# Optimization experiments

Hardware: AMD Instinct MI355X
Metric: run time of the kernel (lower is better)

The kernel has to match this reference:

```python
import jax, jax.numpy as jnp
import numpy as np

BATCH, SEQ, IN_DIM, UNITS = 32, 512, 512, 1024


def setup_inputs() -> dict:
    key = jax.random.key(0)
    k1, k2, k3 = jax.random.split(key, 3)
    data = jax.random.normal(k1, (BATCH, SEQ, IN_DIM), dtype=jnp.float32)
    Wx = jax.random.normal(k2, (IN_DIM, 4 * UNITS), dtype=jnp.float32) * 0.02
    Wh = jax.random.normal(k3, (UNITS, 4 * UNITS), dtype=jnp.float32) * 0.02
    b = jnp.zeros((4 * UNITS,), dtype=jnp.float32)
    return {"data": data, "Wx": Wx, "Wh": Wh, "b": b}


def reference(data, Wx, Wh, b):
    # Precompute input projections for all timesteps at once: [B, T, 4U]
    x_proj = jnp.einsum("bti,iu->btu", data, Wx) + b
    units = Wh.shape[0]
    B = data.shape[0]

    def step(carry, xp_t):
        h, c = carry
        gates = xp_t + h @ Wh  # [B, 4U]
        i, f, g, o = jnp.split(gates, 4, axis=-1)
        i = jax.nn.sigmoid(i)
        f = jax.nn.sigmoid(f)
        g = jnp.tanh(g)
        o = jax.nn.sigmoid(o)
        c_new = f * c + i * g
        h_new = o * jnp.tanh(c_new)
        return (h_new, c_new), h_new

    h0 = jnp.zeros((B, units), dtype=data.dtype)
    c0 = jnp.zeros((B, units), dtype=data.dtype)
    # scan over time axis: xs is [T, B, 4U]
    (_, _), hs = jax.lax.scan(step, (h0, c0), jnp.swapaxes(x_proj, 0, 1))
    # return_sequences=True -> [B, T, U]
    return jnp.swapaxes(hs, 0, 1)
```

## Files before the change

kernel.cpp:

```cpp
#include <hip/hip_runtime.h>
#include <cstdint>
#include <cstddef>

typedef __bf16 bf16x8 __attribute__((ext_vector_type(8)));
typedef __bf16 bf16x4 __attribute__((ext_vector_type(4)));
typedef float  f32x4  __attribute__((ext_vector_type(4)));

#define WS_WFRAG   0
#define WS_XB      12582912
#define WS_XCHG    29360128
#define WS_CNT     62914560
#define WS_NEEDED  62930944

#define LDS_BYTES  163840

#define SENT 0xFFFFFFFFFFFFFFFFULL

__device__ __forceinline__ void gload16(const void* g, void* l) {
    __builtin_amdgcn_global_load_lds(
        (const __attribute__((address_space(1))) void*)(g),
        (__attribute__((address_space(3))) void*)(l),
        16, 0, 0);
}

__device__ __forceinline__ float sigmoidf_(float x) {
    return 1.f / (1.f + __expf(-x));
}
__device__ __forceinline__ float tanhf_(float x) {
    x = fminf(fmaxf(x, -15.f), 15.f);
    float e2 = __expf(2.f * x);
    return (e2 - 1.f) / (e2 + 1.f);
}

__global__ void __launch_bounds__(256) prep_w_kernel(const float* __restrict__ Wx,
                                                     const float* __restrict__ Wh,
                                                     __bf16* __restrict__ wfrag) {
    int tid = blockIdx.x * 256 + threadIdx.x;
    int l   = tid & 63;
    int m   = tid >> 6;
    int nt  = m & 1;
    int sk  = m >> 1;
    int kk  = sk % 48;
    int s   = sk / 48;
    int lc  = l & 15;
    int c   = nt * 16 + lc;
    int uu  = c >> 2;
    int gi  = c & 3;
    int n   = gi * 1024 + s * 8 + uu;
    int k0  = kk * 32 + (l >> 4) * 8;
    bf16x8 v;
#pragma unroll
    for (int j = 0; j < 8; ++j) {
        int k  = k0 + j;
        float f = (k < 512) ? Wx[k * 4096 + n] : Wh[(k - 512) * 4096 + n];
        v[j] = (__bf16)f;
    }
    ((bf16x8*)wfrag)[tid] = v;
}

__global__ void __launch_bounds__(256) prep_x_kernel(const float* __restrict__ data,
                                                     __bf16* __restrict__ xb) {
    int tid = blockIdx.x * 256 + threadIdx.x;
    float4 v = ((const float4*)data)[tid];
    bf16x4 o;
    o[0] = (__bf16)v.x; o[1] = (__bf16)v.y; o[2] = (__bf16)v.z; o[3] = (__bf16)v.w;
    ((bf16x4*)xb)[tid] = o;
}

__global__ void __launch_bounds__(128)
lstm_main(const __bf16* __restrict__ xb, const __bf16* __restrict__ wfrag,
          const float* __restrict__ bias, float* __restrict__ out,
          __bf16* __restrict__ hbuf, unsigned* __restrict__ cnt) {
    extern __shared__ char smem[];
    __bf16* X_lds = (__bf16*)smem;
    __bf16* H_lds = (__bf16*)(smem + 32768);
    __bf16* W_lds = (__bf16*)(smem + 65536);

    const int tid = threadIdx.x;
    const int l   = tid & 63;
    const int w   = tid >> 6;
    const int q   = l >> 4;
    const int r   = l & 15;
    const int bid = blockIdx.x;
    const int s   = bid & 127;
    const int g   = bid >> 7;
    const int gb0 = g * 16;

    const __bf16* wsrc = wfrag + (size_t)s * 49152;
    for (int m = w * 48; m < w * 48 + 48; ++m) {
        gload16(wsrc + m * 512 + l * 8, W_lds + m * 512);
    }

    const int uu = w * 4 + q;
    const int u  = s * 8 + uu;
    const float b_i = bias[u];
    const float b_f = bias[1024 + u];
    const float b_g = bias[2048 + u];
    const float b_o = bias[3072 + u];
    float cst = 0.f;

    unsigned* fl = cnt + g * 1024;

    {
        const __bf16* xrow = xb + (size_t)(gb0 + r) * 512 * 512;
#pragma unroll
        for (int j = 0; j < 8; ++j) {
            int m = w * 8 + j;
            gload16(xrow + m * 32 + q * 8, X_lds + m * 512);
        }
    }

    __syncthreads();

    for (int t = 0; t < 512; ++t) {
        if (t > 0) {
            const unsigned tgt = (unsigned)t;
            while (__hip_atomic_load(fl + w * 64 + l, __ATOMIC_RELAXED,
                                     __HIP_MEMORY_SCOPE_AGENT) < tgt) {}
        }

        unsigned long long va[16], vb[16];
        const __bf16* hsrc = hbuf + (size_t)t * 32768 + (size_t)g * 16384;
#pragma unroll
        for (int j = 0; j < 16; ++j) {
            int m = w * 16 + j;
            ulonglong2 v = *(const ulonglong2*)(hsrc + (m * 4 + q) * 128 + r * 8);
            va[j] = v.x; vb[j] = v.y;
        }

        const __bf16* Xc = X_lds + (t & 1) * 8192;
        f32x4 acc0 = {0.f, 0.f, 0.f, 0.f};
        f32x4 acc1 = {0.f, 0.f, 0.f, 0.f};
#pragma unroll
        for (int kk = 0; kk < 16; kk += 2) {
            bf16x8 a0 = *(const bf16x8*)(Xc + kk * 512 + l * 8);
            bf16x8 b0 = *(const bf16x8*)(W_lds + (kk * 2 + w) * 512 + l * 8);
            acc0 = __builtin_amdgcn_mfma_f32_16x16x32_bf16(a0, b0, acc0, 0, 0, 0);
            bf16x8 a1 = *(const bf16x8*)(Xc + (kk + 1) * 512 + l * 8);
            bf16x8 b1 = *(const bf16x8*)(W_lds + ((kk + 1) * 2 + w) * 512 + l * 8);
            acc1 = __builtin_amdgcn_mfma_f32_16x16x32_bf16(a1, b1, acc1, 0, 0, 0);
        }

        if (t > 0) {
            for (;;) {
                int miss = 0;
#pragma unroll
                for (int j = 0; j < 16; ++j)
                    miss += (va[j] == SENT) + (vb[j] == SENT);
                if (miss == 0) break;
                __builtin_amdgcn_s_sleep(1);
#pragma unroll
                for (int j = 0; j < 16; ++j) {
                    int m = w * 16 + j;
                    const unsigned long long* p =
                        (const unsigned long long*)(hsrc + (m * 4 + q) * 128 + r * 8);
                    if (va[j] == SENT)
                        va[j] = __hip_atomic_load(p,     __ATOMIC_RELAXED, __HIP_MEMORY_SCOPE_AGENT);
                    if (vb[j] == SENT)
                        vb[j] = __hip_atomic_load(p + 1, __ATOMIC_RELAXED, __HIP_MEMORY_SCOPE_AGENT);
                }
            }
        }

#pragma unroll
        for (int j = 0; j < 16; ++j) {
            int m = w * 16 + j;
            unsigned long long tmp[2] = {va[j], vb[j]};
            *((ulonglong2*)(H_lds + m * 512 + l * 8)) = *(const ulonglong2*)tmp;
        }
        __syncthreads();

#pragma unroll 4
        for (int kk = 16; kk < 48; kk += 2) {
            bf16x8 a0 = *(const bf16x8*)(H_lds + (kk - 16) * 512 + l * 8);
            bf16x8 b0 = *(const bf16x8*)(W_lds + (kk * 2 + w) * 512 + l * 8);
            acc0 = __builtin_amdgcn_mfma_f32_16x16x32_bf16(a0, b0, acc0, 0, 0, 0);
            bf16x8 a1 = *(const bf16x8*)(H_lds + (kk - 15) * 512 + l * 8);
            bf16x8 b1 = *(const bf16x8*)(W_lds + ((kk + 1) * 2 + w) * 512 + l * 8);
            acc1 = __builtin_amdgcn_mfma_f32_16x16x32_bf16(a1, b1, acc1, 0, 0, 0);
        }

        float*  scr   = (float*)(smem + ((t + 1) & 1) * 16384);
        __bf16* hpack = (__bf16*)(smem + ((t + 1) & 1) * 16384 + 2176);
        float* sw = scr + w * 272;
#pragma unroll
        for (int rg = 0; rg < 4; ++rg) {
            sw[(l & 15) * 17 + q * 4 + rg] = acc0[rg] + acc1[rg];
        }
        float xi = sw[(q * 4 + 0) * 17 + r];
        float xf = sw[(q * 4 + 1) * 17 + r];
        float xg = sw[(q * 4 + 2) * 17 + r];
        float xo = sw[(q * 4 + 3) * 17 + r];

        float ii = sigmoidf_(xi + b_i);
        float ff = sigmoidf_(xf + b_f);
        float gg = tanhf_(xg + b_g);
        float oo = sigmoidf_(xo + b_o);
        cst = ff * cst + ii * gg;
        float h = oo * tanhf_(cst);

        const int bglob = gb0 + r;

        if (t < 511) {
            hpack[r * 8 + uu] = (__bf16)h;
            __syncthreads();
            if (w == 0) {
                if (tid < 32) {
                    unsigned long long v = ((const unsigned long long*)hpack)[tid];
                    unsigned long long* dst = (unsigned long long*)
                        (hbuf + (size_t)(t + 1) * 32768 + (size_t)g * 16384 + s * 128) + tid;
                    __hip_atomic_store(dst, v, __ATOMIC_RELAXED, __HIP_MEMORY_SCOPE_AGENT);
                }
                if (tid == 0) {
                    __hip_atomic_store(fl + s, (unsigned)(t + 1), __ATOMIC_RELAXED,
                                       __HIP_MEMORY_SCOPE_AGENT);
                }
            }
            out[((size_t)bglob * 512 + t) * 1024 + u] = h;
            {
                const __bf16* xrow = xb + ((size_t)(gb0 + r) * 512 + (t + 1)) * 512;
                __bf16* Xn = X_lds + ((t + 1) & 1) * 8192;
#pragma unroll
                for (int j = 0; j < 8; ++j) {
                    int m = w * 8 + j;
                    gload16(xrow + m * 32 + q * 8, Xn + m * 512);
                }
            }
        } else {
            out[((size_t)bglob * 512 + t) * 1024 + u] = h;
        }
    }
}

extern "C" void kernel_launch(void* const* d_in, const int* in_sizes, int n_in,
                              void* d_out, int out_size, void* d_ws, size_t ws_size,
                              hipStream_t stream) {
    const float* data = (const float*)d_in[0];
    const float* Wx   = (const float*)d_in[1];
    const float* Wh   = (const float*)d_in[2];
    const float* b    = (const float*)d_in[3];
    float* out = (float*)d_out;

    if (ws_size < (size_t)WS_NEEDED) return;

    char* ws = (char*)d_ws;
    __bf16*   wfrag = (__bf16*)(ws + WS_WFRAG);
    __bf16*   xbuf  = (__bf16*)(ws + WS_XB);
    __bf16*   xchg  = (__bf16*)(ws + WS_XCHG);
    unsigned* cnt   = (unsigned*)(ws + WS_CNT);

    hipFuncSetAttribute((const void*)lstm_main,
                        hipFuncAttributeMaxDynamicSharedMemorySize, LDS_BYTES);

    prep_w_kernel<<<3072, 256, 0, stream>>>(Wx, Wh, wfrag);
    prep_x_kernel<<<8192, 256, 0, stream>>>(data, xbuf);
    hipMemsetAsync(ws + WS_XCHG, 0x00, 65536, stream);
    hipMemsetAsync(ws + WS_XCHG + 65536, 0xFF, 33554432 - 65536, stream);
    hipMemsetAsync(ws + WS_CNT,  0x00, 16384, stream);

    lstm_main<<<256, 128, LDS_BYTES, stream>>>(xbuf, wfrag, b, out, xchg, cnt);
}
```

Baseline: 2.055 ms.

## Replace per-block step flags with sharded atomic counters and prefetch h early

Each block used to publish its step with a store to a per-slice flag, and every lane polled all 128 flags before loading h. Now each block atomically increments one of 8 sharded counters per batch group. Thread 0 spins until the counters sum to 128*(t+1), then a block barrier follows. The next step's h loads are issued before that wait, so they can overlap, and the existing sentinel check still retries any stale entries. This cuts flag polling traffic, but adds a fetch_add contention point and a serialising block barrier every step.

```diff
diff --git a/kernel.cpp b/kernel.cpp
--- a/kernel.cpp
+++ b/kernel.cpp
@@ -10,7 +10,7 @@
 #define WS_XB      12582912
 #define WS_XCHG    29360128
 #define WS_CNT     62914560
-#define WS_NEEDED  62930944
+#define WS_NEEDED  62918656
 
 #define LDS_BYTES  163840
 
@@ -99,7 +99,8 @@
     const float b_o = bias[3072 + u];
     float cst = 0.f;
 
-    unsigned* fl = cnt + g * 1024;
+    unsigned* cbase = cnt + g * 512;
+    unsigned* mycnt = cbase + (s & 7) * 64;
 
     {
         const __bf16* xrow = xb + (size_t)(gb0 + r) * 512 * 512;
@@ -110,24 +111,19 @@
         }
     }
 
-    __syncthreads();
-
-    for (int t = 0; t < 512; ++t) {
-        if (t > 0) {
-            const unsigned tgt = (unsigned)t;
-            while (__hip_atomic_load(fl + w * 64 + l, __ATOMIC_RELAXED,
-                                     __HIP_MEMORY_SCOPE_AGENT) < tgt) {}
-        }
-
-        unsigned long long va[16], vb[16];
-        const __bf16* hsrc = hbuf + (size_t)t * 32768 + (size_t)g * 16384;
+    ulonglong2 hv[16];
+    {
+        const __bf16* hsrc = hbuf + (size_t)g * 16384;
 #pragma unroll
         for (int j = 0; j < 16; ++j) {
             int m = w * 16 + j;
-            ulonglong2 v = *(const ulonglong2*)(hsrc + (m * 4 + q) * 128 + r * 8);
-            va[j] = v.x; vb[j] = v.y;
-        }
-
+            hv[j] = *(const ulonglong2*)(hsrc + (m * 4 + q) * 128 + r * 8);
+        }
+    }
+
+    __syncthreads();
+
+    for (int t = 0; t < 512; ++t) {
         const __bf16* Xc = X_lds + (t & 1) * 8192;
         f32x4 acc0 = {0.f, 0.f, 0.f, 0.f};
         f32x4 acc1 = {0.f, 0.f, 0.f, 0.f};
@@ -142,22 +138,23 @@
         }
 
         if (t > 0) {
+            const __bf16* hsrc = hbuf + (size_t)t * 32768 + (size_t)g * 16384;
             for (;;) {
                 int miss = 0;
 #pragma unroll
                 for (int j = 0; j < 16; ++j)
-                    miss += (va[j] == SENT) + (vb[j] == SENT);
+                    miss += (hv[j].x == SENT) + (hv[j].y == SENT);
                 if (miss == 0) break;
-                __builtin_amdgcn_s_sleep(1);
+                __builtin_amdgcn_s_sleep(2);
 #pragma unroll
                 for (int j = 0; j < 16; ++j) {
                     int m = w * 16 + j;
                     const unsigned long long* p =
                         (const unsigned long long*)(hsrc + (m * 4 + q) * 128 + r * 8);
-                    if (va[j] == SENT)
-                        va[j] = __hip_atomic_load(p,     __ATOMIC_RELAXED, __HIP_MEMORY_SCOPE_AGENT);
-                    if (vb[j] == SENT)
-                        vb[j] = __hip_atomic_load(p + 1, __ATOMIC_RELAXED, __HIP_MEMORY_SCOPE_AGENT);
+                    if (hv[j].x == SENT)
+                        hv[j].x = __hip_atomic_load(p,     __ATOMIC_RELAXED, __HIP_MEMORY_SCOPE_AGENT);
+                    if (hv[j].y == SENT)
+                        hv[j].y = __hip_atomic_load(p + 1, __ATOMIC_RELAXED, __HIP_MEMORY_SCOPE_AGENT);
                 }
             }
         }
@@ -165,8 +162,7 @@
 #pragma unroll
         for (int j = 0; j < 16; ++j) {
             int m = w * 16 + j;
-            unsigned long long tmp[2] = {va[j], vb[j]};
-            *((ulonglong2*)(H_lds + m * 512 + l * 8)) = *(const ulonglong2*)tmp;
+            *((ulonglong2*)(H_lds + m * 512 + l * 8)) = hv[j];
         }
         __syncthreads();
 
@@ -212,8 +208,7 @@
                     __hip_atomic_store(dst, v, __ATOMIC_RELAXED, __HIP_MEMORY_SCOPE_AGENT);
                 }
                 if (tid == 0) {
-                    __hip_atomic_store(fl + s, (unsigned)(t + 1), __ATOMIC_RELAXED,
-                                       __HIP_MEMORY_SCOPE_AGENT);
+                    __hip_atomic_fetch_add(mycnt, 1u, __ATOMIC_RELAXED, __HIP_MEMORY_SCOPE_AGENT);
                 }
             }
             out[((size_t)bglob * 512 + t) * 1024 + u] = h;
@@ -226,6 +221,27 @@
                     gload16(xrow + m * 32 + q * 8, Xn + m * 512);
                 }
             }
+            {
+                const __bf16* hn = hbuf + (size_t)(t + 1) * 32768 + (size_t)g * 16384;
+#pragma unroll
+                for (int j = 0; j < 16; ++j) {
+                    int m = w * 16 + j;
+                    hv[j] = *(const ulonglong2*)(hn + (m * 4 + q) * 128 + r * 8);
+                }
+            }
+            __builtin_amdgcn_sched_barrier(0);
+            if (tid == 0) {
+                const unsigned target = 128u * (unsigned)(t + 1);
+                for (;;) {
+                    unsigned sum = 0;
+#pragma unroll
+                    for (int i = 0; i < 8; ++i)
+                        sum += __hip_atomic_load(cbase + i * 64, __ATOMIC_RELAXED,
+                                                 __HIP_MEMORY_SCOPE_AGENT);
+                    if (sum >= target) break;
+                }
+            }
+            __syncthreads();
         } else {
             out[((size_t)bglob * 512 + t) * 1024 + u] = h;
         }
@@ -256,7 +272,7 @@
     prep_x_kernel<<<8192, 256, 0, stream>>>(data, xbuf);
     hipMemsetAsync(ws + WS_XCHG, 0x00, 65536, stream);
     hipMemsetAsync(ws + WS_XCHG + 65536, 0xFF, 33554432 - 65536, stream);
-    hipMemsetAsync(ws + WS_CNT,  0x00, 16384, stream);
+    hipMemsetAsync(ws + WS_CNT,  0x00, 4096, stream);
 
     lstm_main<<<256, 128, LDS_BYTES, stream>>>(xbuf, wfrag, b, out, xchg, cnt);
 }
```

New measurement: 2.418 ms. 17.7% more time.
